# Performance work log

Hardware: AMD Instinct MI355X
Metric: run time of the kernel (lower is better)

## Reference

```python
import jax, jax.numpy as jnp
import numpy as np

D = 64        # emb_size
L = 4         # n_layers
ND = 4        # directions per layer: v2c, c2v, v2k, k2v
N_VAR, N_CONS, N_CUT = 100000, 50000, 20000
E_VC, E_VK = 800000, 200000
EF = 8        # edge feature dim
LN_EPS = 1e-3  # keras LayerNormalization default epsilon


def mlp2(x, w1, b1, w2, b2):
    # Dense(relu) -> Dense(linear); dropout is identity (training=False)
    return jax.nn.relu(x @ w1 + b1) @ w2 + b2


def layer_norm(x, g, b):
    m = jnp.mean(x, axis=-1, keepdims=True)
    v = jnp.var(x, axis=-1, keepdims=True)
    return (x - m) * jax.lax.rsqrt(v + LN_EPS) * g + b


def message_pass(node, neigh, src, dst, ew, P, i):
    """One MessagePassingLayer. P is a tuple of stacked [16,...] params, i the layer index."""
    (mw1, mb1, mw2, mb2, gw, gb, uw1, ub1, uw2, ub2, lg, lb) = P
    msg = mlp2(neigh, mw1[i], mb1[i], mw2[i], mb2[i])          # [N_src, D]
    wm = msg[src] * ew                                          # [E, D] gather + weight
    n = node.shape[0]
    agg = jax.ops.segment_sum(wm, dst, num_segments=n)          # scatter_nd sum
    deg = jax.ops.segment_sum(ew, dst, num_segments=n)          # [n, 1]
    agg = agg / jnp.maximum(deg, 1.0)
    comb = jnp.concatenate([agg, node], axis=-1)                # [n, 2D]
    gate = jax.nn.sigmoid(comb @ gw[i] + gb[i])
    upd = mlp2(comb, uw1[i], ub1[i], uw2[i], ub2[i])
    out = gate * upd + (1.0 - gate) * node
    return layer_norm(out, lg[i], lb[i])


def edge_weight(src_f, dst_f, e_f, w1, b1, w2, b2):
    comb = jnp.concatenate([src_f, dst_f, e_f], axis=-1)
    return jax.nn.sigmoid(jax.nn.relu(comb @ w1 + b1) @ w2 + b2)  # [E, 1]


def setup_inputs() -> dict:
    keys = iter(jax.random.split(jax.random.key(0), 64))

    def p(shape, scale=0.05):
        return jax.random.normal(next(keys), shape, dtype=jnp.float32) * scale

    inp = {
        'variable_features': jax.random.normal(next(keys), (N_VAR, 19), dtype=jnp.float32),
        'constraint_features': jax.random.normal(next(keys), (N_CONS, 5), dtype=jnp.float32),
        'cut_features': jax.random.normal(next(keys), (N_CUT, 30), dtype=jnp.float32),
        'var_cons_edge_features': jax.random.normal(next(keys), (E_VC, EF), dtype=jnp.float32),
        'var_cut_edge_features': jax.random.normal(next(keys), (E_VK, EF), dtype=jnp.float32),
        'var_cons_edges': jnp.stack([
            jax.random.randint(next(keys), (E_VC,), 0, N_VAR, dtype=jnp.int32),
            jax.random.randint(next(keys), (E_VC,), 0, N_CONS, dtype=jnp.int32)]),
        'var_cut_edges': jnp.stack([
            jax.random.randint(next(keys), (E_VK,), 0, N_VAR, dtype=jnp.int32),
            jax.random.randint(next(keys), (E_VK,), 0, N_CUT, dtype=jnp.int32)]),
    }
    # embedding MLPs
    for name, din in [('var', 19), ('cons', 5), ('cut', 30)]:
        inp[f'{name}_w1'] = p((din, D)); inp[f'{name}_b1'] = p((D,))
        inp[f'{name}_w2'] = p((D, D));  inp[f'{name}_b2'] = p((D,))
    # edge weight modules (input 2D + edge_feat)
    for name in ['ewvc', 'ewvk']:
        inp[f'{name}_w1'] = p((2 * D + EF, D)); inp[f'{name}_b1'] = p((D,))
        inp[f'{name}_w2'] = p((D, 1));          inp[f'{name}_b2'] = p((1,))
    # 16 message passing layers, stacked; index = layer*4 + direction(v2c,c2v,v2k,k2v)
    NL = L * ND
    inp['mp_msg_w1'] = p((NL, D, D));  inp['mp_msg_b1'] = p((NL, D))
    inp['mp_msg_w2'] = p((NL, D, D));  inp['mp_msg_b2'] = p((NL, D))
    inp['mp_gate_w'] = p((NL, 2 * D, D)); inp['mp_gate_b'] = p((NL, D))
    inp['mp_upd_w1'] = p((NL, 2 * D, D)); inp['mp_upd_b1'] = p((NL, D))
    inp['mp_upd_w2'] = p((NL, D, D));  inp['mp_upd_b2'] = p((NL, D))
    inp['mp_ln_g'] = jnp.ones((NL, D), dtype=jnp.float32)
    inp['mp_ln_b'] = jnp.zeros((NL, D), dtype=jnp.float32)
    return inp


def reference(variable_features, constraint_features, cut_features,
              var_cons_edge_features, var_cut_edge_features,
              var_w1, var_b1, var_w2, var_b2,
              cons_w1, cons_b1, cons_w2, cons_b2,
              cut_w1, cut_b1, cut_w2, cut_b2,
              ewvc_w1, ewvc_b1, ewvc_w2, ewvc_b2,
              ewvk_w1, ewvk_b1, ewvk_w2, ewvk_b2,
              mp_msg_w1, mp_msg_b1, mp_msg_w2, mp_msg_b2,
              mp_gate_w, mp_gate_b, mp_upd_w1, mp_upd_b1,
              mp_upd_w2, mp_upd_b2, mp_ln_g, mp_ln_b,
              var_cons_edges, var_cut_edges):
    h_var = mlp2(variable_features, var_w1, var_b1, var_w2, var_b2)
    h_cons = mlp2(constraint_features, cons_w1, cons_b1, cons_w2, cons_b2)
    h_cut = mlp2(cut_features, cut_w1, cut_b1, cut_w2, cut_b2)

    vc_s, vc_d = var_cons_edges[0], var_cons_edges[1]
    vk_s, vk_d = var_cut_edges[0], var_cut_edges[1]

    vc_w = edge_weight(h_var[vc_s], h_cons[vc_d], var_cons_edge_features,
                       ewvc_w1, ewvc_b1, ewvc_w2, ewvc_b2)
    vk_w = edge_weight(h_var[vk_s], h_cut[vk_d], var_cut_edge_features,
                       ewvk_w1, ewvk_b1, ewvk_w2, ewvk_b2)

    P = (mp_msg_w1, mp_msg_b1, mp_msg_w2, mp_msg_b2, mp_gate_w, mp_gate_b,
         mp_upd_w1, mp_upd_b1, mp_upd_w2, mp_upd_b2, mp_ln_g, mp_ln_b)

    for l in range(L):
        h_cons = message_pass(h_cons, h_var, vc_s, vc_d, vc_w, P, l * ND + 0)
        h_var = message_pass(h_var, h_cons, vc_d, vc_s, vc_w, P, l * ND + 1)  # reverse
        h_cut = message_pass(h_cut, h_var, vk_s, vk_d, vk_w, P, l * ND + 2)
        h_var = message_pass(h_var, h_cut, vk_d, vk_s, vk_w, P, l * ND + 3)  # reverse
    return h_cut
```

## Files before the change

kernel.cpp:

```cpp
#include <hip/hip_runtime.h>

#define DEVINL static __device__ __forceinline__

namespace {

typedef __attribute__((ext_vector_type(8))) short bf16x8;
typedef __attribute__((ext_vector_type(4))) float f32x4;

constexpr int NV = 100000;
constexpr int NC = 50000;
constexpr int NK = 20000;
constexpr int EVC = 800000;
constexpr int EVK = 200000;
constexpr int E_TOT2 = 2 * (EVC + EVK);
constexpr int R_TOT = NC + NV + NK + NV;
constexpr int SCAN_CHUNK = 2048;
constexpr int SCAN_NB = (R_TOT + SCAN_CHUNK - 1) / SCAN_CHUNK;
constexpr int PACK_PER_LAYER = 28672;
constexpr float WQ_SCALE = 16383.0f;
constexpr float WQ_INV = 1.0f / 16383.0f;

__constant__ int c_bin_hi[8] = {12500, 25000, 37500, 50000,
                                83334, 116667, 150000, 270000};
__constant__ int c_seg_lo[8] = {0, 0, 0, 0, EVC, EVC, EVC, 2 * EVC};
__constant__ int c_seg_hi[8] = {EVC, EVC, EVC, EVC,
                                2 * EVC, 2 * EVC, 2 * EVC, E_TOT2};

constexpr int PE_VAR_W1 = 0;
constexpr int PE_VAR_W2 = 2048;
constexpr int PE_CONS_W1 = 6144;
constexpr int PE_CONS_W2 = 8192;
constexpr int PE_CUT_W1 = 12288;
constexpr int PE_CUT_W2 = 14336;
constexpr int PE_EWVC_A = 18432;
constexpr int PE_EWVC_B = 22528;
constexpr int PE_EWVK_A = 26624;
constexpr int PE_EWVK_B = 30720;
constexpr int PE_TOTAL = 34816;

DEVINL unsigned short f2bf(float f) {
  unsigned u = __float_as_uint(f);
  u = u + 0x7fffu + ((u >> 16) & 1u);
  return (unsigned short)(u >> 16);
}
DEVINL float bf2f(unsigned short h) {
  return __uint_as_float((unsigned)h << 16);
}

DEVINL float sigmoid_f(float x) { return 1.0f / (1.0f + __expf(-x)); }

DEVINL void pack_mat(const float* __restrict__ src, int K, int Kpad,
                     unsigned short* __restrict__ dst, int tid) {
  const int ntup = (Kpad / 32) * 256;
  for (int tup = tid; tup < ntup; tup += 256) {
    const int lane = tup & 63;
    const int t = (tup >> 6) & 3;
    const int kb = tup >> 8;
    const int c = t * 16 + (lane & 15);
    const int k0 = kb * 32 + (lane >> 4) * 8;
#pragma unroll
    for (int jj = 0; jj < 8; ++jj)
      dst[tup * 8 + jj] =
          (k0 + jj < K) ? f2bf(src[(k0 + jj) * 64 + c]) : (unsigned short)0;
  }
}

__global__ void __launch_bounds__(256) pack_k(
    const float* __restrict__ mW1, const float* __restrict__ mW2,
    const float* __restrict__ gW, const float* __restrict__ uW1,
    const float* __restrict__ uW2, unsigned short* __restrict__ PW) {
  const int layer = blockIdx.x;
  unsigned short* out = PW + (size_t)layer * PACK_PER_LAYER;
  pack_mat(mW1 + (size_t)layer * 4096, 64, 64, out, threadIdx.x);
  pack_mat(mW2 + (size_t)layer * 4096, 64, 64, out + 4096, threadIdx.x);
  pack_mat(gW + (size_t)layer * 8192, 128, 128, out + 8192, threadIdx.x);
  pack_mat(uW1 + (size_t)layer * 8192, 128, 128, out + 16384, threadIdx.x);
  pack_mat(uW2 + (size_t)layer * 4096, 64, 64, out + 24576, threadIdx.x);
}

__global__ void __launch_bounds__(256) pack_emb_k(
    const float* __restrict__ var_w1, const float* __restrict__ var_w2,
    const float* __restrict__ cons_w1, const float* __restrict__ cons_w2,
    const float* __restrict__ cut_w1, const float* __restrict__ cut_w2,
    const float* __restrict__ ewvc_w1, const float* __restrict__ ewvk_w1,
    unsigned short* __restrict__ P) {
  switch (blockIdx.x) {
    case 0: pack_mat(var_w1, 19, 32, P + PE_VAR_W1, threadIdx.x); break;
    case 1: pack_mat(var_w2, 64, 64, P + PE_VAR_W2, threadIdx.x); break;
    case 2: pack_mat(cons_w1, 5, 32, P + PE_CONS_W1, threadIdx.x); break;
    case 3: pack_mat(cons_w2, 64, 64, P + PE_CONS_W2, threadIdx.x); break;
    case 4: pack_mat(cut_w1, 30, 32, P + PE_CUT_W1, threadIdx.x); break;
    case 5: pack_mat(cut_w2, 64, 64, P + PE_CUT_W2, threadIdx.x); break;
    case 6: pack_mat(ewvc_w1, 64, 64, P + PE_EWVC_A, threadIdx.x); break;
    case 7: pack_mat(ewvc_w1 + 64 * 64, 64, 64, P + PE_EWVC_B, threadIdx.x); break;
    case 8: pack_mat(ewvk_w1, 64, 64, P + PE_EWVK_A, threadIdx.x); break;
    case 9: pack_mat(ewvk_w1 + 64 * 64, 64, 64, P + PE_EWVK_B, threadIdx.x); break;
  }
}

template <int DIN>
__global__ void __launch_bounds__(256) emb_mfma_k(
    const float* __restrict__ X, const unsigned short* __restrict__ W1p_,
    const unsigned short* __restrict__ W2p_, const float* __restrict__ B1,
    const float* __restrict__ B2, unsigned short* __restrict__ OUTb, int N) {
  __shared__ unsigned short lds[4][16 * 72];
  const int wave = threadIdx.x >> 6, l = threadIdx.x & 63;
  const int col = l & 15, quad = l >> 4;
  const int n0_raw = blockIdx.x * 64 + wave * 16;
  const bool dead = n0_raw >= N;
  const int n0 = dead ? 0 : n0_raw;

  bf16x8 a0;
#pragma unroll
  for (int j = 0; j < 8; ++j) {
    const int k = quad * 8 + j;
    a0[j] = (k < DIN) ? (short)f2bf(X[(size_t)(n0 + col) * DIN + k]) : (short)0;
  }
  const bf16x8* W1p = (const bf16x8*)W1p_;
  const bf16x8* W2p = (const bf16x8*)W2p_;
  f32x4 acc[4];
#pragma unroll
  for (int t = 0; t < 4; ++t) {
    const float b = B1[col + 16 * t];
    acc[t] = f32x4{b, b, b, b};
  }
#pragma unroll
  for (int t = 0; t < 4; ++t)
    acc[t] = __builtin_amdgcn_mfma_f32_16x16x32_bf16(a0, W1p[t * 64 + l], acc[t], 0, 0, 0);
  unsigned short* ld = lds[wave];
#pragma unroll
  for (int t = 0; t < 4; ++t)
#pragma unroll
    for (int r = 0; r < 4; ++r)
      ld[(quad * 4 + r) * 72 + col + 16 * t] = f2bf(fmaxf(acc[t][r], 0.0f));
  __syncthreads();
  const bf16x8 h0 = *(const bf16x8*)&ld[col * 72 + quad * 8];
  const bf16x8 h1 = *(const bf16x8*)&ld[col * 72 + 32 + quad * 8];
  f32x4 o[4];
#pragma unroll
  for (int t = 0; t < 4; ++t) {
    const float b = B2[col + 16 * t];
    o[t] = f32x4{b, b, b, b};
  }
#pragma unroll
  for (int t = 0; t < 4; ++t) {
    o[t] = __builtin_amdgcn_mfma_f32_16x16x32_bf16(h0, W2p[t * 64 + l], o[t], 0, 0, 0);
    o[t] = __builtin_amdgcn_mfma_f32_16x16x32_bf16(h1, W2p[(4 + t) * 64 + l], o[t], 0, 0, 0);
  }
  __syncthreads();
#pragma unroll
  for (int t = 0; t < 4; ++t)
#pragma unroll
    for (int r = 0; r < 4; ++r)
      ld[(quad * 4 + r) * 72 + col + 16 * t] = f2bf(o[t][r]);
  __syncthreads();
  if (!dead) {
#pragma unroll
    for (int cc = 0; cc < 2; ++cc) {
      const bf16x8 v = *(const bf16x8*)&ld[col * 72 + (quad * 2 + cc) * 8];
      *(bf16x8*)(OUTb + (size_t)(n0 + col) * 64 + (quad * 2 + cc) * 8) = v;
    }
  }
}

template <int NOUT>
__global__ void __launch_bounds__(256) gemv_mfma_k(
    const unsigned short* __restrict__ Xb, const unsigned short* __restrict__ WpA_,
    const unsigned short* __restrict__ WpB_, const float* __restrict__ Bias,
    unsigned short* __restrict__ OUT0, unsigned short* __restrict__ OUT1, int N) {
  __shared__ unsigned short lds[4][16 * 72];
  const int wave = threadIdx.x >> 6, l = threadIdx.x & 63;
  const int col = l & 15, quad = l >> 4;
  const int n0_raw = blockIdx.x * 64 + wave * 16;
  const bool dead = n0_raw >= N;
  const int n0 = dead ? 0 : n0_raw;
  const unsigned short* xrow = Xb + (size_t)(n0 + col) * 64 + quad * 8;
  const bf16x8 a0 = *(const bf16x8*)xrow;
  const bf16x8 a1 = *(const bf16x8*)(xrow + 32);
  unsigned short* ld = lds[wave];
#pragma unroll
  for (int m = 0; m < NOUT; ++m) {
    const bf16x8* Wp = (const bf16x8*)(m == 0 ? WpA_ : WpB_);
    unsigned short* OUT = (m == 0) ? OUT0 : OUT1;
    f32x4 acc[4];
#pragma unroll
    for (int t = 0; t < 4; ++t) {
      const float b = (Bias != nullptr) ? Bias[col + 16 * t] : 0.0f;
      acc[t] = f32x4{b, b, b, b};
    }
#pragma unroll
    for (int t = 0; t < 4; ++t) {
      acc[t] = __builtin_amdgcn_mfma_f32_16x16x32_bf16(a0, Wp[t * 64 + l], acc[t], 0, 0, 0);
      acc[t] = __builtin_amdgcn_mfma_f32_16x16x32_bf16(a1, Wp[(4 + t) * 64 + l], acc[t], 0, 0, 0);
    }
    if (m > 0) __syncthreads();
#pragma unroll
    for (int t = 0; t < 4; ++t)
#pragma unroll
      for (int r = 0; r < 4; ++r)
        ld[(quad * 4 + r) * 72 + col + 16 * t] = f2bf(acc[t][r]);
    __syncthreads();
    if (!dead) {
#pragma unroll
      for (int cc = 0; cc < 2; ++cc) {
        const bf16x8 v = *(const bf16x8*)&ld[col * 72 + (quad * 2 + cc) * 8];
        *(bf16x8*)(OUT + (size_t)(n0 + col) * 64 + (quad * 2 + cc) * 8) = v;
      }
    }
  }
}

__global__ void __launch_bounds__(256) msg_mfma_k(
    const unsigned short* __restrict__ Xb, const unsigned short* __restrict__ Wp,
    const float* __restrict__ B1, const float* __restrict__ B2,
    unsigned short* __restrict__ MSGb, int N) {
  __shared__ unsigned short lds[4][16 * 72];
  const int wave = threadIdx.x >> 6, l = threadIdx.x & 63;
  const int col = l & 15, quad = l >> 4;
  const int n0_raw = blockIdx.x * 64 + wave * 16;
  const bool dead = n0_raw >= N;
  const int n0 = dead ? 0 : n0_raw;

  const unsigned short* xrow = Xb + (size_t)(n0 + col) * 64 + quad * 8;
  const bf16x8 a0 = *(const bf16x8*)xrow;
  const bf16x8 a1 = *(const bf16x8*)(xrow + 32);
  const bf16x8* W1p = (const bf16x8*)Wp;
  const bf16x8* W2p = (const bf16x8*)(Wp + 4096);

  f32x4 acc[4];
#pragma unroll
  for (int t = 0; t < 4; ++t) {
    const float b = B1[col + 16 * t];
    acc[t] = f32x4{b, b, b, b};
  }
#pragma unroll
  for (int t = 0; t < 4; ++t) {
    acc[t] = __builtin_amdgcn_mfma_f32_16x16x32_bf16(a0, W1p[t * 64 + l], acc[t], 0, 0, 0);
    acc[t] = __builtin_amdgcn_mfma_f32_16x16x32_bf16(a1, W1p[(4 + t) * 64 + l], acc[t], 0, 0, 0);
  }
  unsigned short* ld = lds[wave];
#pragma unroll
  for (int t = 0; t < 4; ++t)
#pragma unroll
    for (int r = 0; r < 4; ++r)
      ld[(quad * 4 + r) * 72 + col + 16 * t] = f2bf(fmaxf(acc[t][r], 0.0f));
  __syncthreads();
  const bf16x8 h0 = *(const bf16x8*)&ld[col * 72 + quad * 8];
  const bf16x8 h1 = *(const bf16x8*)&ld[col * 72 + 32 + quad * 8];
  f32x4 o[4];
#pragma unroll
  for (int t = 0; t < 4; ++t) {
    const float b = B2[col + 16 * t];
    o[t] = f32x4{b, b, b, b};
  }
#pragma unroll
  for (int t = 0; t < 4; ++t) {
    o[t] = __builtin_amdgcn_mfma_f32_16x16x32_bf16(h0, W2p[t * 64 + l], o[t], 0, 0, 0);
    o[t] = __builtin_amdgcn_mfma_f32_16x16x32_bf16(h1, W2p[(4 + t) * 64 + l], o[t], 0, 0, 0);
  }
  __syncthreads();
#pragma unroll
  for (int t = 0; t < 4; ++t)
#pragma unroll
    for (int r = 0; r < 4; ++r)
      ld[(quad * 4 + r) * 72 + col + 16 * t] = f2bf(o[t][r]);
  __syncthreads();
  if (!dead) {
#pragma unroll
    for (int cc = 0; cc < 2; ++cc) {
      const bf16x8 v = *(const bf16x8*)&ld[col * 72 + (quad * 2 + cc) * 8];
      *(bf16x8*)(MSGb + (size_t)(n0 + col) * 64 + (quad * 2 + cc) * 8) = v;
    }
  }
}

template <int WITH_MSG>
__global__ void __launch_bounds__(256) pass_mfma_k(
    const int* __restrict__ row_ptr, const unsigned* __restrict__ adj,
    const float* __restrict__ degi, const unsigned short* __restrict__ MSGsrc,
    const unsigned short* __restrict__ NODEb,
    const unsigned short* __restrict__ gWp, const unsigned short* __restrict__ uW1p,
    const unsigned short* __restrict__ uW2p, const float* __restrict__ gB,
    const float* __restrict__ uB1, const float* __restrict__ uB2,
    const float* __restrict__ LNG, const float* __restrict__ LNB,
    const unsigned short* __restrict__ mWp,
    const float* __restrict__ mB1, const float* __restrict__ mB2,
    float* __restrict__ OUTf, unsigned short* __restrict__ OUTb,
    unsigned short* __restrict__ MSGdst, int base, int N) {
  __shared__ unsigned short lds[4][16 * 72];
  const int wave = threadIdx.x >> 6, l = threadIdx.x & 63;
  const int col = l & 15, quad = l >> 4;
  const int n0_raw = blockIdx.x * 64 + wave * 16;
  const bool dead = n0_raw >= N;
  const int n0 = dead ? 0 : n0_raw;

  const int r = base + n0 + col;
  const int ps = row_ptr[r], pe = row_ptr[r + 1];
  float acc0[8], acc1[8];
#pragma unroll
  for (int j = 0; j < 8; ++j) { acc0[j] = 0.0f; acc1[j] = 0.0f; }
  int p = ps;
  for (; p + 4 <= pe; p += 4) {
    unsigned av[4];
#pragma unroll
    for (int j = 0; j < 4; ++j) av[j] = adj[p + j];
    bf16x8 m0[4], m1[4];
#pragma unroll
    for (int j = 0; j < 4; ++j) {
      const unsigned short* m = MSGsrc + (size_t)(av[j] >> 14) * 64 + quad * 8;
      m0[j] = *(const bf16x8*)m;
      m1[j] = *(const bf16x8*)(m + 32);
    }
#pragma unroll
    for (int j = 0; j < 4; ++j) {
      const float w = (float)(av[j] & 16383u) * WQ_INV;
      const unsigned* u0 = (const unsigned*)&m0[j];
      const unsigned* u1 = (const unsigned*)&m1[j];
#pragma unroll
      for (int q = 0; q < 4; ++q) {
        acc0[2 * q] = fmaf(__uint_as_float(u0[q] << 16), w, acc0[2 * q]);
        acc0[2 * q + 1] = fmaf(__uint_as_float(u0[q] & 0xffff0000u), w, acc0[2 * q + 1]);
        acc1[2 * q] = fmaf(__uint_as_float(u1[q] << 16), w, acc1[2 * q]);
        acc1[2 * q + 1] = fmaf(__uint_as_float(u1[q] & 0xffff0000u), w, acc1[2 * q + 1]);
      }
    }
  }
  for (; p + 2 <= pe; p += 2) {
    const unsigned avA = adj[p], avB = adj[p + 1];
    const unsigned short* mA = MSGsrc + (size_t)(avA >> 14) * 64 + quad * 8;
    const unsigned short* mB = MSGsrc + (size_t)(avB >> 14) * 64 + quad * 8;
    const bf16x8 mA0 = *(const bf16x8*)mA;
    const bf16x8 mA1 = *(const bf16x8*)(mA + 32);
    const bf16x8 mB0 = *(const bf16x8*)mB;
    const bf16x8 mB1v = *(const bf16x8*)(mB + 32);
    const float wA = (float)(avA & 16383u) * WQ_INV;
    const float wB = (float)(avB & 16383u) * WQ_INV;
    const unsigned* uA0 = (const unsigned*)&mA0;
    const unsigned* uA1 = (const unsigned*)&mA1;
    const unsigned* uB0 = (const unsigned*)&mB0;
    const unsigned* uB1v = (const unsigned*)&mB1v;
#pragma unroll
    for (int q = 0; q < 4; ++q) {
      acc0[2 * q] = fmaf(__uint_as_float(uA0[q] << 16), wA, acc0[2 * q]);
      acc0[2 * q + 1] = fmaf(__uint_as_float(uA0[q] & 0xffff0000u), wA, acc0[2 * q + 1]);
      acc1[2 * q] = fmaf(__uint_as_float(uA1[q] << 16), wA, acc1[2 * q]);
      acc1[2 * q + 1] = fmaf(__uint_as_float(uA1[q] & 0xffff0000u), wA, acc1[2 * q + 1]);
      acc0[2 * q] = fmaf(__uint_as_float(uB0[q] << 16), wB, acc0[2 * q]);
      acc0[2 * q + 1] = fmaf(__uint_as_float(uB0[q] & 0xffff0000u), wB, acc0[2 * q + 1]);
      acc1[2 * q] = fmaf(__uint_as_float(uB1v[q] << 16), wB, acc1[2 * q]);
      acc1[2 * q + 1] = fmaf(__uint_as_float(uB1v[q] & 0xffff0000u), wB, acc1[2 * q + 1]);
    }
  }
  if (p < pe) {
    const unsigned av = adj[p];
    const unsigned short* m = MSGsrc + (size_t)(av >> 14) * 64 + quad * 8;
    const bf16x8 m0 = *(const bf16x8*)m;
    const bf16x8 m1 = *(const bf16x8*)(m + 32);
    const float w = (float)(av & 16383u) * WQ_INV;
    const unsigned* u0 = (const unsigned*)&m0;
    const unsigned* u1 = (const unsigned*)&m1;
#pragma unroll
    for (int q = 0; q < 4; ++q) {
      acc0[2 * q] = fmaf(__uint_as_float(u0[q] << 16), w, acc0[2 * q]);
      acc0[2 * q + 1] = fmaf(__uint_as_float(u0[q] & 0xffff0000u), w, acc0[2 * q + 1]);
      acc1[2 * q] = fmaf(__uint_as_float(u1[q] << 16), w, acc1[2 * q]);
      acc1[2 * q + 1] = fmaf(__uint_as_float(u1[q] & 0xffff0000u), w, acc1[2 * q + 1]);
    }
  }
  const float di = degi[r];
  bf16x8 aA0, aA1;
#pragma unroll
  for (int j = 0; j < 8; ++j) {
    aA0[j] = (short)f2bf(acc0[j] * di);
    aA1[j] = (short)f2bf(acc1[j] * di);
  }

  const unsigned short* nrow = NODEb + (size_t)(n0 + col) * 64 + quad * 8;
  const bf16x8 aN0 = *(const bf16x8*)nrow;
  const bf16x8 aN1 = *(const bf16x8*)(nrow + 32);
  const bf16x8* gW = (const bf16x8*)gWp;
  const bf16x8* uW1 = (const bf16x8*)uW1p;
  const bf16x8* uW2 = (const bf16x8*)uW2p;

  f32x4 g[4], u[4];
#pragma unroll
  for (int t = 0; t < 4; ++t) {
    const float bg = gB[col + 16 * t], bu = uB1[col + 16 * t];
    g[t] = f32x4{bg, bg, bg, bg};
    u[t] = f32x4{bu, bu, bu, bu};
  }
#pragma unroll
  for (int t = 0; t < 4; ++t) {
    g[t] = __builtin_amdgcn_mfma_f32_16x16x32_bf16(aA0, gW[t * 64 + l], g[t], 0, 0, 0);
    g[t] = __builtin_amdgcn_mfma_f32_16x16x32_bf16(aA1, gW[(4 + t) * 64 + l], g[t], 0, 0, 0);
    g[t] = __builtin_amdgcn_mfma_f32_16x16x32_bf16(aN0, gW[(8 + t) * 64 + l], g[t], 0, 0, 0);
    g[t] = __builtin_amdgcn_mfma_f32_16x16x32_bf16(aN1, gW[(12 + t) * 64 + l], g[t], 0, 0, 0);
    u[t] = __builtin_amdgcn_mfma_f32_16x16x32_bf16(aA0, uW1[t * 64 + l], u[t], 0, 0, 0);
    u[t] = __builtin_amdgcn_mfma_f32_16x16x32_bf16(aA1, uW1[(4 + t) * 64 + l], u[t], 0, 0, 0);
    u[t] = __builtin_amdgcn_mfma_f32_16x16x32_bf16(aN0, uW1[(8 + t) * 64 + l], u[t], 0, 0, 0);
    u[t] = __builtin_amdgcn_mfma_f32_16x16x32_bf16(aN1, uW1[(12 + t) * 64 + l], u[t], 0, 0, 0);
  }
#pragma unroll
  for (int t = 0; t < 4; ++t)
#pragma unroll
    for (int r2 = 0; r2 < 4; ++r2) g[t][r2] = sigmoid_f(g[t][r2]);

  unsigned short* ld = lds[wave];
#pragma unroll
  for (int t = 0; t < 4; ++t)
#pragma unroll
    for (int r2 = 0; r2 < 4; ++r2)
      ld[(quad * 4 + r2) * 72 + col + 16 * t] = f2bf(fmaxf(u[t][r2], 0.0f));
  __syncthreads();
  const bf16x8 h0 = *(const bf16x8*)&ld[col * 72 + quad * 8];
  const bf16x8 h1 = *(const bf16x8*)&ld[col * 72 + 32 + quad * 8];
  f32x4 o[4];
#pragma unroll
  for (int t = 0; t < 4; ++t) {
    const float b = uB2[col + 16 * t];
    o[t] = f32x4{b, b, b, b};
  }
#pragma unroll
  for (int t = 0; t < 4; ++t) {
    o[t] = __builtin_amdgcn_mfma_f32_16x16x32_bf16(h0, uW2[t * 64 + l], o[t], 0, 0, 0);
    o[t] = __builtin_amdgcn_mfma_f32_16x16x32_bf16(h1, uW2[(4 + t) * 64 + l], o[t], 0, 0, 0);
  }
  float om[4][4];
#pragma unroll
  for (int t = 0; t < 4; ++t)
#pragma unroll
    for (int r2 = 0; r2 < 4; ++r2) {
      const float nd =
          bf2f(NODEb[(size_t)(n0 + quad * 4 + r2) * 64 + col + 16 * t]);
      om[t][r2] = fmaf(g[t][r2], o[t][r2] - nd, nd);
    }
  float outv[4][4];
#pragma unroll
  for (int r2 = 0; r2 < 4; ++r2) {
    float s1 = (om[0][r2] + om[1][r2]) + (om[2][r2] + om[3][r2]);
    float s2 = fmaf(om[0][r2], om[0][r2], fmaf(om[1][r2], om[1][r2],
                fmaf(om[2][r2], om[2][r2], om[3][r2] * om[3][r2])));
#pragma unroll
    for (int off = 1; off < 16; off <<= 1) {
      s1 += __shfl_xor(s1, off, 64);
      s2 += __shfl_xor(s2, off, 64);
    }
    const float m = s1 * (1.0f / 64.0f);
    const float var = s2 * (1.0f / 64.0f) - m * m;
    const float rr = rsqrtf(var + 1e-3f);
#pragma unroll
    for (int t = 0; t < 4; ++t)
      outv[t][r2] = fmaf((om[t][r2] - m) * rr, LNG[col + 16 * t], LNB[col + 16 * t]);
  }
  if (OUTf != nullptr && !dead) {
#pragma unroll
    for (int t = 0; t < 4; ++t)
#pragma unroll
      for (int r2 = 0; r2 < 4; ++r2)
        OUTf[(size_t)(n0 + quad * 4 + r2) * 64 + col + 16 * t] = outv[t][r2];
  }
  __syncthreads();
#pragma unroll
  for (int t = 0; t < 4; ++t)
#pragma unroll
    for (int r2 = 0; r2 < 4; ++r2)
      ld[(quad * 4 + r2) * 72 + col + 16 * t] = f2bf(outv[t][r2]);
  __syncthreads();
  if (OUTb != nullptr && !dead) {
#pragma unroll
    for (int cc = 0; cc < 2; ++cc) {
      const bf16x8 v = *(const bf16x8*)&ld[col * 72 + (quad * 2 + cc) * 8];
      *(bf16x8*)(OUTb + (size_t)(n0 + col) * 64 + (quad * 2 + cc) * 8) = v;
    }
  }

  if constexpr (WITH_MSG) {
    const bf16x8 x0 = *(const bf16x8*)&ld[col * 72 + quad * 8];
    const bf16x8 x1 = *(const bf16x8*)&ld[col * 72 + 32 + quad * 8];
    const bf16x8* W1p = (const bf16x8*)mWp;
    const bf16x8* W2p = (const bf16x8*)(mWp + 4096);
    f32x4 macc[4];
#pragma unroll
    for (int t = 0; t < 4; ++t) {
      const float b = mB1[col + 16 * t];
      macc[t] = f32x4{b, b, b, b};
    }
#pragma unroll
    for (int t = 0; t < 4; ++t) {
      macc[t] = __builtin_amdgcn_mfma_f32_16x16x32_bf16(x0, W1p[t * 64 + l], macc[t], 0, 0, 0);
      macc[t] = __builtin_amdgcn_mfma_f32_16x16x32_bf16(x1, W1p[(4 + t) * 64 + l], macc[t], 0, 0, 0);
    }
    __syncthreads();
#pragma unroll
    for (int t = 0; t < 4; ++t)
#pragma unroll
      for (int r2 = 0; r2 < 4; ++r2)
        ld[(quad * 4 + r2) * 72 + col + 16 * t] = f2bf(fmaxf(macc[t][r2], 0.0f));
    __syncthreads();
    const bf16x8 mh0 = *(const bf16x8*)&ld[col * 72 + quad * 8];
    const bf16x8 mh1 = *(const bf16x8*)&ld[col * 72 + 32 + quad * 8];
    f32x4 mo[4];
#pragma unroll
    for (int t = 0; t < 4; ++t) {
      const float b = mB2[col + 16 * t];
      mo[t] = f32x4{b, b, b, b};
    }
#pragma unroll
    for (int t = 0; t < 4; ++t) {
      mo[t] = __builtin_amdgcn_mfma_f32_16x16x32_bf16(mh0, W2p[t * 64 + l], mo[t], 0, 0, 0);
      mo[t] = __builtin_amdgcn_mfma_f32_16x16x32_bf16(mh1, W2p[(4 + t) * 64 + l], mo[t], 0, 0, 0);
    }
    __syncthreads();
#pragma unroll
    for (int t = 0; t < 4; ++t)
#pragma unroll
      for (int r2 = 0; r2 < 4; ++r2)
        ld[(quad * 4 + r2) * 72 + col + 16 * t] = f2bf(mo[t][r2]);
    __syncthreads();
    if (!dead) {
#pragma unroll
      for (int cc = 0; cc < 2; ++cc) {
        const bf16x8 v = *(const bf16x8*)&ld[col * 72 + (quad * 2 + cc) * 8];
        *(bf16x8*)(MSGdst + (size_t)(n0 + col) * 64 + (quad * 2 + cc) * 8) = v;
      }
    }
  }
}

__global__ void __launch_bounds__(256) edgew_k(
    const int* __restrict__ S, const int* __restrict__ D,
    const float* __restrict__ EFX, const unsigned short* __restrict__ PA,
    const unsigned short* __restrict__ PB, const float* __restrict__ W1C,
    const float* __restrict__ W2, const float* __restrict__ B2,
    unsigned long long* __restrict__ stagedD,
    unsigned long long* __restrict__ stagedS,
    int* __restrict__ counts, int baseD, int baseS, int E) {
  const int l = threadIdx.x & 63;
  const int g = l >> 3, c = l & 7;
  float wc[8][8];
#pragma unroll
  for (int i = 0; i < 8; ++i) {
    const float4 v0 = *(const float4*)(W1C + i * 64 + c * 8);
    const float4 v1 = *(const float4*)(W1C + i * 64 + c * 8 + 4);
    wc[i][0] = v0.x; wc[i][1] = v0.y; wc[i][2] = v0.z; wc[i][3] = v0.w;
    wc[i][4] = v1.x; wc[i][5] = v1.y; wc[i][6] = v1.z; wc[i][7] = v1.w;
  }
  float w2c[8];
  {
    const float4 a0 = *(const float4*)(W2 + c * 8);
    const float4 a1 = *(const float4*)(W2 + c * 8 + 4);
    w2c[0] = a0.x; w2c[1] = a0.y; w2c[2] = a0.z; w2c[3] = a0.w;
    w2c[4] = a1.x; w2c[5] = a1.y; w2c[6] = a1.z; w2c[7] = a1.w;
  }
  const float b2 = B2[0];
  const int wave_id = blockIdx.x * 4 + (threadIdx.x >> 6);
  const int nwaves = gridDim.x * 4;
  for (int t0 = wave_id * 8; t0 < E; t0 += nwaves * 8) {
    const int e = t0 + g;
    const bool ok = e < E;
    const int ee = ok ? e : E - 1;
    const int s = __builtin_nontemporal_load(S + ee);
    const int d = __builtin_nontemporal_load(D + ee);
    int kd = 0, ks = 0;
    const int rd = baseD + d, rs = baseS + s;
    if (ok && c == 0) {
      kd = atomicAdd(&counts[rd], 1);
      ks = atomicAdd(&counts[rs], 1);
    }
    const bf16x8 pa = *(const bf16x8*)(PA + (size_t)s * 64 + c * 8);
    const bf16x8 pb = *(const bf16x8*)(PB + (size_t)d * 64 + c * 8);
    const f32x4 ef0 =
        __builtin_nontemporal_load((const f32x4*)(EFX + (size_t)ee * 8));
    const f32x4 ef1 =
        __builtin_nontemporal_load((const f32x4*)(EFX + (size_t)ee * 8 + 4));
    const unsigned* pau = (const unsigned*)&pa;
    const unsigned* pbu = (const unsigned*)&pb;
    float h[8];
#pragma unroll
    for (int q = 0; q < 4; ++q) {
      h[2 * q] = __uint_as_float(pau[q] << 16) + __uint_as_float(pbu[q] << 16);
      h[2 * q + 1] = __uint_as_float(pau[q] & 0xffff0000u) +
                     __uint_as_float(pbu[q] & 0xffff0000u);
    }
    const float ef[8] = {ef0[0], ef0[1], ef0[2], ef0[3],
                         ef1[0], ef1[1], ef1[2], ef1[3]};
#pragma unroll
    for (int i = 0; i < 8; ++i)
#pragma unroll
      for (int j = 0; j < 8; ++j) h[j] = fmaf(ef[i], wc[i][j], h[j]);
    float t = 0.0f;
#pragma unroll
    for (int j = 0; j < 8; ++j) t = fmaf(fmaxf(h[j], 0.0f), w2c[j], t);
#pragma unroll
    for (int off = 1; off < 8; off <<= 1) t += __shfl_xor(t, off, 64);
    if (ok && c == 0) {
      const float w = sigmoid_f(t + b2);
      const unsigned w14 = (unsigned)(w * WQ_SCALE + 0.5f);
      stagedD[e] =
          (unsigned long long)((unsigned)rd | ((unsigned)kd << 19)) |
          ((unsigned long long)(((unsigned)s << 14) | w14) << 32);
      stagedS[e] =
          (unsigned long long)((unsigned)rs | ((unsigned)ks << 19)) |
          ((unsigned long long)(((unsigned)d << 14) | w14) << 32);
    }
  }
}

__global__ void __launch_bounds__(256) fill_staged_k(
    const unsigned long long* __restrict__ staged,
    const int* __restrict__ row_ptr, unsigned* __restrict__ adj) {
  const int bin = blockIdx.x & 7;
  const int blk = blockIdx.x >> 3;
  const int nblk = gridDim.x >> 3;
  const int lo = (bin == 0) ? 0 : c_bin_hi[bin - 1];
  const int hi = c_bin_hi[bin];
  const int slo = c_seg_lo[bin], shi = c_seg_hi[bin];
  for (int i = slo + blk * 256 + threadIdx.x; i < shi; i += nblk * 256) {
    const unsigned long long v = __builtin_nontemporal_load(staged + i);
    const int row = (int)(v & 0x7ffffull);
    if (row >= lo && row < hi) {
      const int k = (int)((v >> 19) & 0x1fffull);
      adj[row_ptr[row] + k] = (unsigned)(v >> 32);
    }
  }
}

__global__ void __launch_bounds__(256) degi_k(const int* __restrict__ row_ptr,
                                             const unsigned* __restrict__ adj,
                                             float* __restrict__ degi) {
  const int r = blockIdx.x * 256 + threadIdx.x;
  if (r >= R_TOT) return;
  const int s = row_ptr[r], e = row_ptr[r + 1];
  float d = 0.0f;
  for (int p = s; p < e; ++p) d += (float)(adj[p] & 16383u) * WQ_INV;
  degi[r] = 1.0f / fmaxf(d, 1.0f);
}

__global__ void __launch_bounds__(256) scan1_k(const int* __restrict__ in,
                                               int* __restrict__ bsum) {
  __shared__ int sd[256];
  const int t = threadIdx.x;
  const int base = blockIdx.x * SCAN_CHUNK + t * 8;
  int s = 0;
#pragma unroll
  for (int i = 0; i < 8; ++i) {
    const int idx = base + i;
    s += (idx < R_TOT) ? in[idx] : 0;
  }
  sd[t] = s;
  __syncthreads();
  for (int off = 128; off > 0; off >>= 1) {
    if (t < off) sd[t] += sd[t + off];
    __syncthreads();
  }
  if (t == 0) bsum[blockIdx.x] = sd[0];
}

__global__ void __launch_bounds__(256) scan2_k(int* __restrict__ bsum,
                                               int* __restrict__ row_ptr) {
  __shared__ int sd[256];
  const int t = threadIdx.x;
  const int v = (t < SCAN_NB) ? bsum[t] : 0;
  sd[t] = v;
  __syncthreads();
  for (int off = 1; off < 256; off <<= 1) {
    const int add = (t >= off) ? sd[t - off] : 0;
    __syncthreads();
    sd[t] += add;
    __syncthreads();
  }
  if (t < SCAN_NB) bsum[t] = sd[t] - v;
  if (t == 255) row_ptr[R_TOT] = sd[255];
}

__global__ void __launch_bounds__(256) scan3_k(const int* __restrict__ in,
                                               const int* __restrict__ bsum,
                                               int* __restrict__ out) {
  __shared__ int sd[256];
  const int t = threadIdx.x;
  const int base = blockIdx.x * SCAN_CHUNK + t * 8;
  int loc[8];
  int s = 0;
#pragma unroll
  for (int i = 0; i < 8; ++i) {
    loc[i] = s;
    const int idx = base + i;
    s += (idx < R_TOT) ? in[idx] : 0;
  }
  sd[t] = s;
  __syncthreads();
  const int v = s;
  for (int off = 1; off < 256; off <<= 1) {
    const int add = (t >= off) ? sd[t - off] : 0;
    __syncthreads();
    sd[t] += add;
    __syncthreads();
  }
  const int off0 = bsum[blockIdx.x] + (sd[t] - v);
#pragma unroll
  for (int i = 0; i < 8; ++i) {
    const int idx = base + i;
    if (idx < R_TOT) out[idx] = off0 + loc[i];
  }
}

}

extern "C" void kernel_launch(void* const* d_in, const int* in_sizes, int n_in,
                              void* d_out, int out_size, void* d_ws, size_t ws_size,
                              hipStream_t stream) {
  (void)in_sizes; (void)n_in; (void)out_size; (void)ws_size;

  const float* variable_features   = (const float*)d_in[0];
  const float* constraint_features = (const float*)d_in[1];
  const float* cut_features        = (const float*)d_in[2];
  const float* vc_ef = (const float*)d_in[3];
  const float* vk_ef = (const float*)d_in[4];
  const int* vc_edges = (const int*)d_in[5];
  const int* vk_edges = (const int*)d_in[6];
  const int *vc_s = vc_edges, *vc_d = vc_edges + EVC;
  const int *vk_s = vk_edges, *vk_d = vk_edges + EVK;
  const float* var_w1  = (const float*)d_in[7];
  const float* var_b1  = (const float*)d_in[8];
  const float* var_w2  = (const float*)d_in[9];
  const float* var_b2  = (const float*)d_in[10];
  const float* cons_w1 = (const float*)d_in[11];
  const float* cons_b1 = (const float*)d_in[12];
  const float* cons_w2 = (const float*)d_in[13];
  const float* cons_b2 = (const float*)d_in[14];
  const float* cut_w1  = (const float*)d_in[15];
  const float* cut_b1  = (const float*)d_in[16];
  const float* cut_w2  = (const float*)d_in[17];
  const float* cut_b2  = (const float*)d_in[18];
  const float* ewvc_w1 = (const float*)d_in[19];
  const float* ewvc_b1 = (const float*)d_in[20];
  const float* ewvc_w2 = (const float*)d_in[21];
  const float* ewvc_b2 = (const float*)d_in[22];
  const float* ewvk_w1 = (const float*)d_in[23];
  const float* ewvk_b1 = (const float*)d_in[24];
  const float* ewvk_w2 = (const float*)d_in[25];
  const float* ewvk_b2 = (const float*)d_in[26];
  const float* mp_msg_w1 = (const float*)d_in[27];
  const float* mp_msg_b1 = (const float*)d_in[28];
  const float* mp_msg_w2 = (const float*)d_in[29];
  const float* mp_msg_b2 = (const float*)d_in[30];
  const float* mp_gate_w = (const float*)d_in[31];
  const float* mp_gate_b = (const float*)d_in[32];
  const float* mp_upd_w1 = (const float*)d_in[33];
  const float* mp_upd_b1 = (const float*)d_in[34];
  const float* mp_upd_w2 = (const float*)d_in[35];
  const float* mp_upd_b2 = (const float*)d_in[36];
  const float* mp_ln_g   = (const float*)d_in[37];
  const float* mp_ln_b   = (const float*)d_in[38];

  char* wp = (char*)d_ws;
  auto take = [&](size_t nbytes) {
    char* p = wp;
    wp += (nbytes + 255) & ~(size_t)255;
    return p;
  };
  unsigned short* h_var_b  = (unsigned short*)take((size_t)NV * 64 * 2);
  unsigned short* h_cons_b = (unsigned short*)take((size_t)NC * 64 * 2);
  unsigned short* h_cut_b  = (unsigned short*)take((size_t)NK * 64 * 2);
  unsigned short* msg_ping = (unsigned short*)take((size_t)NV * 64 * 2);
  unsigned short* msg_pong = (unsigned short*)take((size_t)NV * 64 * 2);
  unsigned short* pa = (unsigned short*)take((size_t)NV * 64 * 2);
  unsigned short* pb = (unsigned short*)take((size_t)NC * 64 * 2);
  unsigned short* qa = (unsigned short*)take((size_t)NV * 64 * 2);
  unsigned short* qb = (unsigned short*)take((size_t)NK * 64 * 2);
  unsigned short* packW = (unsigned short*)take((size_t)15 * PACK_PER_LAYER * 2);
  unsigned short* packE = (unsigned short*)take((size_t)PE_TOTAL * 2);
  int* row_ptr = (int*)take((size_t)(R_TOT + 1) * 4);
  int* counts  = (int*)take((size_t)R_TOT * 4);
  int* bsum    = (int*)take(256 * 4);
  float* degi  = (float*)take((size_t)R_TOT * 4);
  unsigned* adj = (unsigned*)take((size_t)(2 * EVC + 2 * EVK) * 4);

  unsigned long long* staged = (unsigned long long*)msg_ping;

  hipMemsetAsync(counts, 0, (size_t)R_TOT * 4, stream);

  pack_k<<<15, 256, 0, stream>>>(mp_msg_w1, mp_msg_w2, mp_gate_w, mp_upd_w1,
                                 mp_upd_w2, packW);
  pack_emb_k<<<10, 256, 0, stream>>>(var_w1, var_w2, cons_w1, cons_w2, cut_w1,
                                     cut_w2, ewvc_w1, ewvk_w1, packE);

  emb_mfma_k<19><<<(NV + 63) / 64, 256, 0, stream>>>(
      variable_features, packE + PE_VAR_W1, packE + PE_VAR_W2, var_b1, var_b2,
      h_var_b, NV);
  emb_mfma_k<5><<<(NC + 63) / 64, 256, 0, stream>>>(
      constraint_features, packE + PE_CONS_W1, packE + PE_CONS_W2, cons_b1,
      cons_b2, h_cons_b, NC);
  emb_mfma_k<30><<<(NK + 63) / 64, 256, 0, stream>>>(
      cut_features, packE + PE_CUT_W1, packE + PE_CUT_W2, cut_b1, cut_b2,
      h_cut_b, NK);

  gemv_mfma_k<2><<<(NV + 63) / 64, 256, 0, stream>>>(
      h_var_b, packE + PE_EWVC_A, packE + PE_EWVK_A, nullptr, pa, qa, NV);
  gemv_mfma_k<1><<<(NC + 63) / 64, 256, 0, stream>>>(
      h_cons_b, packE + PE_EWVC_B, nullptr, ewvc_b1, pb, nullptr, NC);
  gemv_mfma_k<1><<<(NK + 63) / 64, 256, 0, stream>>>(
      h_cut_b, packE + PE_EWVK_B, nullptr, ewvk_b1, qb, nullptr, NK);

  edgew_k<<<1024, 256, 0, stream>>>(vc_s, vc_d, vc_ef, pa, pb,
                                    ewvc_w1 + 128 * 64, ewvc_w2, ewvc_b2,
                                    staged, staged + EVC, counts, 0, NC, EVC);
  edgew_k<<<512, 256, 0, stream>>>(vk_s, vk_d, vk_ef, qa, qb,
                                   ewvk_w1 + 128 * 64, ewvk_w2, ewvk_b2,
                                   staged + 2 * EVC, staged + 2 * EVC + EVK,
                                   counts, NC + NV, NC + NV + NK, EVK);

  scan1_k<<<SCAN_NB, 256, 0, stream>>>(counts, bsum);
  scan2_k<<<1, 256, 0, stream>>>(bsum, row_ptr);
  scan3_k<<<SCAN_NB, 256, 0, stream>>>(counts, bsum, row_ptr);
  fill_staged_k<<<8 * 192, 256, 0, stream>>>(staged, row_ptr, adj);
  degi_k<<<(R_TOT + 255) / 256, 256, 0, stream>>>(row_ptr, adj, degi);

  unsigned short* nodeb_t[4] = {h_cons_b, h_var_b, h_cut_b, h_var_b};
  const int Nd_t[4] = {NC, NV, NK, NV};
  const int base_t[4] = {0, NC, NC + NV, NC + NV + NK};

  msg_mfma_k<<<(NV + 63) / 64, 256, 0, stream>>>(
      h_var_b, packW, mp_msg_b1, mp_msg_b2, msg_ping, NV);

  for (int i = 0; i < 15; ++i) {
    const int d = i & 3;
    const int Nd = Nd_t[d], base = base_t[d];
    const unsigned short* Wl = packW + (size_t)i * PACK_PER_LAYER;
    const unsigned short* src = (i % 2 == 0) ? msg_ping : msg_pong;
    unsigned short* dst = (i % 2 == 0) ? msg_pong : msg_ping;

    if (i < 14) {
      const unsigned short* Wn = packW + (size_t)(i + 1) * PACK_PER_LAYER;
      pass_mfma_k<1><<<(Nd + 63) / 64, 256, 0, stream>>>(
          row_ptr, adj, degi, src, nodeb_t[d], Wl + 8192, Wl + 16384,
          Wl + 24576, mp_gate_b + (size_t)i * 64, mp_upd_b1 + (size_t)i * 64,
          mp_upd_b2 + (size_t)i * 64, mp_ln_g + (size_t)i * 64,
          mp_ln_b + (size_t)i * 64, Wn, mp_msg_b1 + (size_t)(i + 1) * 64,
          mp_msg_b2 + (size_t)(i + 1) * 64, nullptr, nodeb_t[d], dst, base, Nd);
    } else {
      pass_mfma_k<0><<<(Nd + 63) / 64, 256, 0, stream>>>(
          row_ptr, adj, degi, src, nodeb_t[d], Wl + 8192, Wl + 16384,
          Wl + 24576, mp_gate_b + (size_t)i * 64, mp_upd_b1 + (size_t)i * 64,
          mp_upd_b2 + (size_t)i * 64, mp_ln_g + (size_t)i * 64,
          mp_ln_b + (size_t)i * 64, nullptr, nullptr, nullptr,
          (float*)d_out, nullptr, nullptr, base, Nd);
    }
  }
}
```

Measured before the change: 812.2 us.

## Sort destination rows by degree to balance wave-level gather loops

Adds a counting sort of destination rows by in-degree within each of the four row groups, producing a permutation. The fused message-pass kernel processes rows in that order, so the 16 rows sharing a wave have similar edge counts and less divergence in the gather loop. Outputs and node reads use the permuted row indices. The cost is three extra setup kernels, an indirection load per row, and scattered rather than contiguous row writes and reads in the pass kernel.

```diff
diff --git a/kernel.cpp b/kernel.cpp
--- a/kernel.cpp
+++ b/kernel.cpp
@@ -48,6 +48,11 @@
 }
 
 DEVINL float sigmoid_f(float x) { return 1.0f / (1.0f + __expf(-x)); }
+
+DEVINL int row_group(int r) {
+  return (r < NC) ? 0 : (r < NC + NV) ? 1 : (r < NC + NV + NK) ? 2 : 3;
+}
+__constant__ int c_grp_base[4] = {0, NC, NC + NV, NC + NV + NK};
 
 DEVINL void pack_mat(const float* __restrict__ src, int K, int Kpad,
                      unsigned short* __restrict__ dst, int tid) {
@@ -278,7 +283,7 @@
 __global__ void __launch_bounds__(256) pass_mfma_k(
     const int* __restrict__ row_ptr, const unsigned* __restrict__ adj,
     const float* __restrict__ degi, const unsigned short* __restrict__ MSGsrc,
-    const unsigned short* __restrict__ NODEb,
+    const unsigned short* __restrict__ NODEb, const int* __restrict__ perm,
     const unsigned short* __restrict__ gWp, const unsigned short* __restrict__ uW1p,
     const unsigned short* __restrict__ uW2p, const float* __restrict__ gB,
     const float* __restrict__ uB1, const float* __restrict__ uB2,
@@ -294,7 +299,12 @@
   const bool dead = n0_raw >= N;
   const int n0 = dead ? 0 : n0_raw;
 
-  const int r = base + n0 + col;
+  const int lcol = perm[base + n0 + col];
+  int pr[4];
+#pragma unroll
+  for (int j = 0; j < 4; ++j) pr[j] = perm[base + n0 + quad * 4 + j];
+
+  const int r = base + lcol;
   const int ps = row_ptr[r], pe = row_ptr[r + 1];
   float acc0[8], acc1[8];
 #pragma unroll
@@ -375,7 +385,7 @@
     aA1[j] = (short)f2bf(acc1[j] * di);
   }
 
-  const unsigned short* nrow = NODEb + (size_t)(n0 + col) * 64 + quad * 8;
+  const unsigned short* nrow = NODEb + (size_t)lcol * 64 + quad * 8;
   const bf16x8 aN0 = *(const bf16x8*)nrow;
   const bf16x8 aN1 = *(const bf16x8*)(nrow + 32);
   const bf16x8* gW = (const bf16x8*)gWp;
@@ -430,8 +440,7 @@
   for (int t = 0; t < 4; ++t)
 #pragma unroll
     for (int r2 = 0; r2 < 4; ++r2) {
-      const float nd =
-          bf2f(NODEb[(size_t)(n0 + quad * 4 + r2) * 64 + col + 16 * t]);
+      const float nd = bf2f(NODEb[(size_t)pr[r2] * 64 + col + 16 * t]);
       om[t][r2] = fmaf(g[t][r2], o[t][r2] - nd, nd);
     }
   float outv[4][4];
@@ -457,7 +466,7 @@
     for (int t = 0; t < 4; ++t)
 #pragma unroll
       for (int r2 = 0; r2 < 4; ++r2)
-        OUTf[(size_t)(n0 + quad * 4 + r2) * 64 + col + 16 * t] = outv[t][r2];
+        OUTf[(size_t)pr[r2] * 64 + col + 16 * t] = outv[t][r2];
   }
   __syncthreads();
 #pragma unroll
@@ -470,7 +479,7 @@
 #pragma unroll
     for (int cc = 0; cc < 2; ++cc) {
       const bf16x8 v = *(const bf16x8*)&ld[col * 72 + (quad * 2 + cc) * 8];
-      *(bf16x8*)(OUTb + (size_t)(n0 + col) * 64 + (quad * 2 + cc) * 8) = v;
+      *(bf16x8*)(OUTb + (size_t)lcol * 64 + (quad * 2 + cc) * 8) = v;
     }
   }
 
@@ -521,7 +530,7 @@
 #pragma unroll
       for (int cc = 0; cc < 2; ++cc) {
         const bf16x8 v = *(const bf16x8*)&ld[col * 72 + (quad * 2 + cc) * 8];
-        *(bf16x8*)(MSGdst + (size_t)(n0 + col) * 64 + (quad * 2 + cc) * 8) = v;
+        *(bf16x8*)(MSGdst + (size_t)lcol * 64 + (quad * 2 + cc) * 8) = v;
       }
     }
   }
@@ -634,6 +643,44 @@
   float d = 0.0f;
   for (int p = s; p < e; ++p) d += (float)(adj[p] & 16383u) * WQ_INV;
   degi[r] = 1.0f / fmaxf(d, 1.0f);
+}
+
+__global__ void __launch_bounds__(256) dsort1_k(const int* __restrict__ counts,
+                                                int* __restrict__ hist,
+                                                int* __restrict__ kk) {
+  const int r = blockIdx.x * 256 + threadIdx.x;
+  if (r >= R_TOT) return;
+  const int grp = row_group(r);
+  const int bin = min(counts[r], 255);
+  kk[r] = atomicAdd(&hist[grp * 256 + bin], 1);
+}
+__global__ void __launch_bounds__(256) dsort2_k(int* __restrict__ hist) {
+  __shared__ int sd[256];
+  const int t = threadIdx.x;
+  for (int g = 0; g < 4; ++g) {
+    const int v = hist[g * 256 + t];
+    sd[t] = v;
+    __syncthreads();
+    for (int off = 1; off < 256; off <<= 1) {
+      const int add = (t >= off) ? sd[t - off] : 0;
+      __syncthreads();
+      sd[t] += add;
+      __syncthreads();
+    }
+    hist[g * 256 + t] = sd[t] - v;
+    __syncthreads();
+  }
+}
+__global__ void __launch_bounds__(256) dsort3_k(const int* __restrict__ counts,
+                                                const int* __restrict__ hist,
+                                                const int* __restrict__ kk,
+                                                int* __restrict__ perm) {
+  const int r = blockIdx.x * 256 + threadIdx.x;
+  if (r >= R_TOT) return;
+  const int grp = row_group(r);
+  const int bin = min(counts[r], 255);
+  const int gb = c_grp_base[grp];
+  perm[gb + hist[grp * 256 + bin] + kk[r]] = r - gb;
 }
 
 __global__ void __launch_bounds__(256) scan1_k(const int* __restrict__ in,
@@ -773,12 +820,16 @@
   int* row_ptr = (int*)take((size_t)(R_TOT + 1) * 4);
   int* counts  = (int*)take((size_t)R_TOT * 4);
   int* bsum    = (int*)take(256 * 4);
+  int* hist    = (int*)take(1024 * 4);
+  int* kk      = (int*)take((size_t)R_TOT * 4);
+  int* perm    = (int*)take((size_t)R_TOT * 4);
   float* degi  = (float*)take((size_t)R_TOT * 4);
   unsigned* adj = (unsigned*)take((size_t)(2 * EVC + 2 * EVK) * 4);
 
   unsigned long long* staged = (unsigned long long*)msg_ping;
 
   hipMemsetAsync(counts, 0, (size_t)R_TOT * 4, stream);
+  hipMemsetAsync(hist, 0, 1024 * 4, stream);
 
   pack_k<<<15, 256, 0, stream>>>(mp_msg_w1, mp_msg_w2, mp_gate_w, mp_upd_w1,
                                  mp_upd_w2, packW);
@@ -813,6 +864,9 @@
   scan1_k<<<SCAN_NB, 256, 0, stream>>>(counts, bsum);
   scan2_k<<<1, 256, 0, stream>>>(bsum, row_ptr);
   scan3_k<<<SCAN_NB, 256, 0, stream>>>(counts, bsum, row_ptr);
+  dsort1_k<<<(R_TOT + 255) / 256, 256, 0, stream>>>(counts, hist, kk);
+  dsort2_k<<<1, 256, 0, stream>>>(hist);
+  dsort3_k<<<(R_TOT + 255) / 256, 256, 0, stream>>>(counts, hist, kk, perm);
   fill_staged_k<<<8 * 192, 256, 0, stream>>>(staged, row_ptr, adj);
   degi_k<<<(R_TOT + 255) / 256, 256, 0, stream>>>(row_ptr, adj, degi);
 
@@ -833,14 +887,14 @@
     if (i < 14) {
       const unsigned short* Wn = packW + (size_t)(i + 1) * PACK_PER_LAYER;
       pass_mfma_k<1><<<(Nd + 63) / 64, 256, 0, stream>>>(
-          row_ptr, adj, degi, src, nodeb_t[d], Wl + 8192, Wl + 16384,
+          row_ptr, adj, degi, src, nodeb_t[d], perm, Wl + 8192, Wl + 16384,
           Wl + 24576, mp_gate_b + (size_t)i * 64, mp_upd_b1 + (size_t)i * 64,
           mp_upd_b2 + (size_t)i * 64, mp_ln_g + (size_t)i * 64,
           mp_ln_b + (size_t)i * 64, Wn, mp_msg_b1 + (size_t)(i + 1) * 64,
           mp_msg_b2 + (size_t)(i + 1) * 64, nullptr, nodeb_t[d], dst, base, Nd);
     } else {
       pass_mfma_k<0><<<(Nd + 63) / 64, 256, 0, stream>>>(
-          row_ptr, adj, degi, src, nodeb_t[d], Wl + 8192, Wl + 16384,
+          row_ptr, adj, degi, src, nodeb_t[d], perm, Wl + 8192, Wl + 16384,
           Wl + 24576, mp_gate_b + (size_t)i * 64, mp_upd_b1 + (size_t)i * 64,
           mp_upd_b2 + (size_t)i * 64, mp_ln_g + (size_t)i * 64,
           mp_ln_b + (size_t)i * 64, nullptr, nullptr, nullptr,
```

After: 1.381 ms. +70.0%, slower.
